# Performance work log

Measured on AMD Instinct MI355X. Metric: run time of the kernel, lower is better.

Reference implementation:

```python
import jax, jax.numpy as jnp
import numpy as np
from jax import lax

PRE_NMS_TOPK = 6000
POST_NMS_TOPK = 1000
NMS_THRESH = 0.7
MIN_SIZE = 16.0


def setup_inputs() -> dict:
    key = jax.random.key(0)
    k1, k2, k3, k4, k5 = jax.random.split(key, 5)
    B, N = 16, 200000
    # anchors: valid boxes (x1 < x2, y1 < y2) from random centers / sizes
    cxy = jax.random.uniform(k1, (B, N, 2), dtype=jnp.float32) * 1000.0
    wh = 16.0 + jax.random.uniform(k2, (B, N, 2), dtype=jnp.float32) * 284.0
    anchors = jnp.concatenate([cxy - 0.5 * wh, cxy + 0.5 * wh], axis=-1)  # [B,N,4] x1,y1,x2,y2
    image_sizes = jax.random.randint(k3, (B, 2), 512, 1024, dtype=jnp.int32)  # (h, w)
    objectness_logits = jax.random.normal(k4, (B, N, 1), dtype=jnp.float32)
    bbox_deltas = jax.random.normal(k5, (B, N, 4), dtype=jnp.float32) * 0.2
    return {"anchors": anchors, "image_sizes": image_sizes,
            "objectness_logits": objectness_logits, "bbox_deltas": bbox_deltas}


def _per_image(anchors, image_size, logits, deltas):
    # --- box decode ---
    a_w = anchors[:, 2] - anchors[:, 0]
    a_h = anchors[:, 3] - anchors[:, 1]
    a_x = anchors[:, 0] + 0.5 * a_w
    a_y = anchors[:, 1] + 0.5 * a_h
    p_x = a_x + deltas[:, 0] * a_w
    p_y = a_y + deltas[:, 1] * a_h
    p_w = a_w * jnp.exp(jnp.clip(deltas[:, 2], -10.0, 10.0))
    p_h = a_h * jnp.exp(jnp.clip(deltas[:, 3], -10.0, 10.0))
    h = image_size[0].astype(jnp.float32)
    w = image_size[1].astype(jnp.float32)
    x1 = jnp.clip(p_x - 0.5 * p_w, 0.0, w - 1.0)
    y1 = jnp.clip(p_y - 0.5 * p_h, 0.0, h - 1.0)
    x2 = jnp.clip(p_x + 0.5 * p_w, 0.0, w - 1.0)
    y2 = jnp.clip(p_y + 0.5 * p_h, 0.0, h - 1.0)
    proposals = jnp.stack([x1, y1, x2, y2], axis=1)  # [N,4]
    # --- min-size filter (mask instead of gather) ---
    valid = ((x2 - x1) >= MIN_SIZE) & ((y2 - y1) >= MIN_SIZE)
    fg = jax.nn.sigmoid(logits[:, 0])
    fg = jnp.where(valid, fg, -1.0)  # sentinel < 0 marks invalid
    # --- pre-NMS top-k ---
    scores, idx = lax.top_k(fg, PRE_NMS_TOPK)  # descending
    props = proposals[idx]  # [K,4]
    lgt = logits[idx]       # [K,1]
    dlt = deltas[idx]       # [K,4]
    bx1, by1, bx2, by2 = props[:, 0], props[:, 1], props[:, 2], props[:, 3]
    areas = (bx2 - bx1) * (by2 - by1)

    # --- greedy NMS: select highest remaining score, suppress IoU > thresh ---
    def step(sc, _):
        i = jnp.argmax(sc)
        s = sc[i]
        iw = jnp.maximum(0.0, jnp.minimum(bx2, bx2[i]) - jnp.maximum(bx1, bx1[i]))
        ih = jnp.maximum(0.0, jnp.minimum(by2, by2[i]) - jnp.maximum(by1, by1[i]))
        inter = iw * ih
        union = areas + areas[i] - inter
        iou = jnp.where(union > 0.0, inter / jnp.where(union > 0.0, union, 1.0), 0.0)
        sc = jnp.where(iou > NMS_THRESH, -1.0, sc)
        sc = sc.at[i].set(-1.0)
        return sc, (i, s > -0.5)

    _, (keep_idx, keep_valid) = lax.scan(step, scores, None, length=POST_NMS_TOPK)
    vm = keep_valid[:, None]
    out_p = jnp.where(vm, props[keep_idx], 0.0)
    out_l = jnp.where(vm, lgt[keep_idx], 1e-08)
    out_d = jnp.where(vm, dlt[keep_idx], 0.0)
    return out_p, out_l, out_d, keep_valid


def reference(anchors, image_sizes, objectness_logits, bbox_deltas):
    return jax.vmap(_per_image)(anchors, image_sizes, objectness_logits, bbox_deltas)
```

## Files before the change

### kernel.cpp

```cpp
#include <hip/hip_runtime.h>

#define BN 16
#define NN 200000
#define TOPK 6000
#define POSTK 1000
#define MW 285744
#define KEY_NEGHALF 0x40FFFFFFu
#define EQCAP 8192

#pragma clang fp contract(off)

typedef unsigned long long u64;

__device__ __forceinline__ float exp_cr(float x) {
  return (float)exp((double)x);
}

__device__ __forceinline__ unsigned key_of(float s) {
  unsigned u = __float_as_uint(s);
  return (u & 0x80000000u) ? ~u : (u | 0x80000000u);
}

__device__ __forceinline__ void decode_box(float4 a, float4 d, float W1, float H1,
                                           float& x1, float& y1, float& x2, float& y2,
                                           bool& valid) {
  float aw = a.z - a.x;
  float ah = a.w - a.y;
  float ax = a.x + 0.5f * aw;
  float ay = a.y + 0.5f * ah;
  float px = ax + d.x * aw;
  float py = ay + d.y * ah;
  float cz = fminf(fmaxf(d.z, -10.0f), 10.0f);
  float cw = fminf(fmaxf(d.w, -10.0f), 10.0f);
  float pw = aw * exp_cr(cz);
  float ph = ah * exp_cr(cw);
  x1 = fminf(fmaxf(px - 0.5f * pw, 0.0f), W1);
  y1 = fminf(fmaxf(py - 0.5f * ph, 0.0f), H1);
  x2 = fminf(fmaxf(px + 0.5f * pw, 0.0f), W1);
  y2 = fminf(fmaxf(py + 0.5f * ph, 0.0f), H1);
  valid = ((x2 - x1) >= 16.0f) && ((y2 - y1) >= 16.0f);
}

__device__ __forceinline__ float score_of(float lg, bool valid) {
  float e = exp_cr(-lg);
  float s = 1.0f / (1.0f + e);
  return valid ? s : -1.0f;
}

__global__ __launch_bounds__(256) void k_score(const float4* __restrict__ anchors,
                                               const int* __restrict__ isz,
                                               const float* __restrict__ logits,
                                               const float4* __restrict__ deltas,
                                               unsigned* __restrict__ keys,
                                               unsigned* __restrict__ hist0) {
  __shared__ unsigned h[256];
  int b = blockIdx.y;
  int idx = blockIdx.x * 256 + threadIdx.x;
  int lane = threadIdx.x & 63;
  h[threadIdx.x] = 0;
  __syncthreads();
  unsigned bin = 0;
  bool active = idx < NN;
  if (active) {
    size_t i = (size_t)b * NN + idx;
    float4 a = anchors[i];
    float4 d = deltas[i];
    float H1 = (float)isz[2 * b] - 1.0f;
    float W1 = (float)isz[2 * b + 1] - 1.0f;
    float x1, y1, x2, y2; bool valid;
    decode_box(a, d, W1, H1, x1, y1, x2, y2, valid);
    float sc = score_of(logits[i], valid);
    unsigned key = key_of(sc);
    keys[i] = key;
    bin = key >> 24;
  }
  u64 act = __ballot(active);
  while (act) {
    int l = __ffsll(act) - 1;
    unsigned vb = __shfl(bin, l);
    u64 same = __ballot(bin == vb) & act;
    if (lane == l) atomicAdd(&h[vb], (unsigned)__popcll(same));
    act &= ~same;
  }
  __syncthreads();
  unsigned c = h[threadIdx.x];
  if (c) atomicAdd(&hist0[((size_t)b * 8 + (blockIdx.x & 7)) * 256 + threadIdx.x], c);
}

__global__ void k_sel0(const unsigned* __restrict__ hist0, unsigned* __restrict__ meta) {
  int b = blockIdx.x, t = threadIdx.x;
  __shared__ unsigned c[256];
  unsigned s = 0;
  for (int sh = 0; sh < 8; ++sh) s += hist0[((size_t)b * 8 + sh) * 256 + t];
  c[t] = s;
  __syncthreads();
  if (t == 0) {
    unsigned cum = 0;
    for (int u = 255; u >= 0; --u) {
      if (cum + c[u] >= TOPK) { meta[b * 8 + 0] = (unsigned)u; meta[b * 8 + 1] = cum; break; }
      cum += c[u];
    }
  }
}

__global__ __launch_bounds__(256) void k_h1(const unsigned* __restrict__ keys,
                                            const unsigned* __restrict__ meta,
                                            unsigned* __restrict__ hist1) {
  int b = blockIdx.y;
  int idx = blockIdx.x * 256 + threadIdx.x;
  if (idx >= NN) return;
  unsigned key = keys[(size_t)b * NN + idx];
  unsigned B0 = meta[b * 8 + 0];
  if ((key >> 24) == B0)
    atomicAdd(&hist1[(size_t)b * 65536 + ((key >> 8) & 0xFFFFu)], 1u);
}

__global__ void k_sel1(const unsigned* __restrict__ hist1, unsigned* __restrict__ meta) {
  int b = blockIdx.x, t = threadIdx.x;
  __shared__ unsigned part[256];
  __shared__ unsigned above[256];
  const unsigned* h = hist1 + (size_t)b * 65536;
  unsigned cA0 = meta[b * 8 + 1];
  unsigned R1 = TOPK - cA0;
  int base = t * 256;
  unsigned sum = 0;
  for (int j = 0; j < 256; ++j) sum += h[base + j];
  part[t] = sum;
  __syncthreads();
  if (t == 0) {
    unsigned run = 0;
    for (int u = 255; u >= 0; --u) { above[u] = run; run += part[u]; }
  }
  __syncthreads();
  unsigned ab = above[t];
  if (ab < R1 && ab + part[t] >= R1) {
    unsigned cum = ab;
    for (int j = 255; j >= 0; --j) {
      unsigned c = h[base + j];
      if (cum + c >= R1) {
        meta[b * 8 + 2] = (unsigned)(base + j);
        meta[b * 8 + 3] = cA0 + cum;
        break;
      }
      cum += c;
    }
  }
}

__global__ __launch_bounds__(256) void k_h2(const unsigned* __restrict__ keys,
                                            const unsigned* __restrict__ meta,
                                            unsigned* __restrict__ hist2) {
  int b = blockIdx.y;
  int idx = blockIdx.x * 256 + threadIdx.x;
  if (idx >= NN) return;
  unsigned key = keys[(size_t)b * NN + idx];
  unsigned pref = (meta[b * 8 + 0] << 16) | meta[b * 8 + 2];
  if ((key >> 8) == pref)
    atomicAdd(&hist2[b * 256 + (key & 0xFFu)], 1u);
}

__global__ void k_sel2(const unsigned* __restrict__ hist2, unsigned* __restrict__ meta) {
  int b = blockIdx.x, t = threadIdx.x;
  __shared__ unsigned c[256];
  c[t] = hist2[b * 256 + t];
  __syncthreads();
  if (t == 0) {
    unsigned R2 = TOPK - meta[b * 8 + 3];
    unsigned cum = 0;
    for (int u = 255; u >= 0; --u) {
      if (cum + c[u] >= R2) {
        unsigned K = (meta[b * 8 + 0] << 24) | (meta[b * 8 + 2] << 8) | (unsigned)u;
        unsigned nG = meta[b * 8 + 3] + cum;
        meta[b * 8 + 4] = K;
        meta[b * 8 + 5] = nG;
        meta[b * 8 + 6] = TOPK - nG;
        break;
      }
      cum += c[u];
    }
  }
}

__global__ __launch_bounds__(256) void k_compact(const unsigned* __restrict__ keys,
                                                 const unsigned* __restrict__ meta,
                                                 unsigned* __restrict__ cntGt,
                                                 unsigned* __restrict__ sel,
                                                 unsigned* __restrict__ cntEq,
                                                 unsigned* __restrict__ eq) {
  __shared__ unsigned sc[256];
  __shared__ unsigned baseSh;
  int b = blockIdx.y, tid = threadIdx.x;
  const unsigned* kb = keys + (size_t)b * NN;
  unsigned K = meta[b * 8 + 4];
  int start = blockIdx.x * 8000;
  int end = start + 8000 < NN ? start + 8000 : NN;
  unsigned cnt = 0;
  for (int n = start + tid; n < end; n += 256) cnt += (kb[n] > K);
  sc[tid] = cnt;
  __syncthreads();
  if (tid == 0) {
    unsigned run = 0;
    for (int u = 0; u < 256; ++u) { unsigned v = sc[u]; sc[u] = run; run += v; }
    baseSh = run ? atomicAdd(&cntGt[b * 64], run) : 0u;
  }
  __syncthreads();
  unsigned pos = baseSh + sc[tid];
  for (int n = start + tid; n < end; n += 256) {
    unsigned kv = kb[n];
    if (kv > K) {
      sel[(size_t)b * TOPK + pos++] = (unsigned)n;
    } else if (kv == K) {
      unsigned p = atomicAdd(&cntEq[b * 64], 1u);
      if (p < EQCAP) eq[(size_t)b * EQCAP + p] = (unsigned)n;
    }
  }
}

__global__ __launch_bounds__(256) void k_resolve2(const unsigned* __restrict__ eq,
                                                  const unsigned* __restrict__ cntEq,
                                                  const unsigned* __restrict__ meta,
                                                  unsigned* __restrict__ sel) {
  __shared__ unsigned lst[EQCAP];
  int b = blockIdx.x, t = threadIdx.x;
  unsigned cnt = cntEq[b * 64];
  if (cnt > EQCAP) cnt = EQCAP;
  unsigned nG = meta[b * 8 + 5], nE = meta[b * 8 + 6];
  for (unsigned j = t; j < cnt; j += 256) lst[j] = eq[(size_t)b * EQCAP + j];
  __syncthreads();
  for (unsigned j = t; j < cnt; j += 256) {
    unsigned my = lst[j];
    unsigned rank = 0;
    for (unsigned k = 0; k < cnt; ++k) rank += (lst[k] < my);
    if (rank < nE) sel[(size_t)b * TOPK + nG + rank] = my;
  }
}

__global__ __launch_bounds__(1024) void k_sort(const float4* __restrict__ anchors,
                                               const int* __restrict__ isz,
                                               const unsigned* __restrict__ keys,
                                               const float4* __restrict__ deltas,
                                               const unsigned* __restrict__ sel,
                                               unsigned* __restrict__ sIdx,
                                               unsigned* __restrict__ sKey,
                                               float4* __restrict__ sBox,
                                               float* __restrict__ sAr) {
  __shared__ u64 skey[8192];
  int b = blockIdx.x, tid = threadIdx.x;
  for (int p = tid; p < 8192; p += 1024) {
    u64 kk = 0;
    if (p < TOPK) {
      unsigned n = sel[(size_t)b * TOPK + p];
      kk = ((u64)keys[(size_t)b * NN + n] << 32) | (unsigned)(NN - 1 - (int)n);
    }
    skey[p] = kk;
  }
  __syncthreads();
  for (unsigned k = 2; k <= 8192; k <<= 1) {
    for (unsigned j = k >> 1; j > 0; j >>= 1) {
      for (unsigned p = tid; p < 4096; p += 1024) {
        unsigned i = ((p & ~(j - 1)) << 1) | (p & (j - 1));
        unsigned x = i | j;
        u64 a = skey[i], c = skey[x];
        bool desc = ((i & k) == 0);
        if (desc ? (a < c) : (a > c)) { skey[i] = c; skey[x] = a; }
      }
      __syncthreads();
    }
  }
  float H1 = (float)isz[2 * b] - 1.0f;
  float W1 = (float)isz[2 * b + 1] - 1.0f;
  for (int i = tid; i < TOPK; i += 1024) {
    u64 kk = skey[i];
    unsigned n = (unsigned)(NN - 1) - (unsigned)(kk & 0xFFFFFFFFull);
    sIdx[(size_t)b * TOPK + i] = n;
    sKey[(size_t)b * TOPK + i] = (unsigned)(kk >> 32);
    float4 a = anchors[(size_t)b * NN + n];
    float4 d = deltas[(size_t)b * NN + n];
    float x1, y1, x2, y2; bool valid;
    decode_box(a, d, W1, H1, x1, y1, x2, y2, valid);
    sBox[(size_t)b * TOPK + i] = make_float4(x1, y1, x2, y2);
    sAr[(size_t)b * TOPK + i] = (x2 - x1) * (y2 - y1);
  }
}

__global__ __launch_bounds__(256) void k_iou(const float4* __restrict__ sBox,
                                             const float* __restrict__ sAr,
                                             u64* __restrict__ mat) {
  int Bk = blockIdx.x;
  int c = blockIdx.y;
  int b = blockIdx.z;
  int wlo = c * 16;
  int whi = wlo + 16 > 94 ? 94 : wlo + 16;
  if (wlo < Bk) wlo = Bk;
  if (wlo >= whi) return;
  int tid = threadIdx.x, wv = tid >> 6, lane = tid & 63;
  __shared__ float4 cb[1024];
  __shared__ float ca[1024];
  __shared__ float4 rb[64];
  __shared__ float ra[64];
  const float4* sb = sBox + (size_t)b * TOPK;
  const float* sa = sAr + (size_t)b * TOPK;
  for (int u = tid; u < 1024; u += 256) {
    int j = c * 1024 + u;
    int jc = j < TOPK ? j : TOPK - 1;
    cb[u] = sb[jc];
    ca[u] = sa[jc];
  }
  if (tid < 64) {
    int i = Bk * 64 + tid;
    int ic = i < TOPK ? i : TOPK - 1;
    rb[tid] = sb[ic];
    ra[tid] = sa[ic];
  }
  __syncthreads();
  const double T = (double)0.7f + 0x1p-25;
  size_t matb = (size_t)b * MW;
  for (int g = 0; g < 4; ++g) {
    int r0 = wv * 16 + g * 4;
    float4 r4[4]; float rar[4]; size_t ro[4]; bool rok[4];
    for (int k = 0; k < 4; ++k) {
      int i = Bk * 64 + r0 + k;
      r4[k] = rb[r0 + k];
      rar[k] = ra[r0 + k];
      rok[k] = i < TOPK;
      int rm = i & 63;
      ro[k] = matb + (size_t)(94 * i - (32 * Bk * (Bk - 1) + Bk * rm)) - (size_t)Bk;
    }
    for (int w = wlo; w < whi; ++w) {
      int u = (w - c * 16) * 64 + lane;
      float4 c4 = cb[u];
      float car = ca[u];
#pragma unroll
      for (int k = 0; k < 4; ++k) {
        if (!rok[k]) continue;
        float iw = fminf(c4.z, r4[k].z) - fmaxf(c4.x, r4[k].x);
        iw = fmaxf(iw, 0.0f);
        float ih = fminf(c4.w, r4[k].w) - fmaxf(c4.y, r4[k].y);
        ih = fmaxf(ih, 0.0f);
        float inter = iw * ih;
        float uni = (car + rar[k]) - inter;
        bool pred = (uni > 0.0f) && ((double)inter >= T * (double)uni);
        u64 w64 = __ballot(pred);
        if (lane == 0) mat[ro[k] + (size_t)w] = w64;
      }
    }
  }
}

__global__ __launch_bounds__(1024) void k_scan(const float4* __restrict__ anchors,
                                               const int* __restrict__ isz,
                                               const float* __restrict__ logits,
                                               const float4* __restrict__ deltas,
                                               const unsigned* __restrict__ sIdx,
                                               const unsigned* __restrict__ sKey,
                                               const u64* __restrict__ mat,
                                               float* __restrict__ out) {
  __shared__ u64 rmW[94];
  __shared__ u64 diagb[2][64];
  __shared__ unsigned keyb[2][64];
  __shared__ unsigned idxb[2][64];
  __shared__ unsigned keepL[POSTK];
  __shared__ unsigned picksList[64];
  __shared__ int nkSh, npicksSh, allInvSh;
  int b = blockIdx.x, tid = threadIdx.x, lane = tid & 63, wv = tid >> 6;
  const u64* mb = mat + (size_t)b * MW;
  const size_t bT = (size_t)b * TOPK;
  if (tid < 94) rmW[tid] = 0;
  if (tid == 0) { nkSh = 0; allInvSh = 0; }
  if (wv == 1) {
    diagb[0][lane] = mb[(size_t)(94 * lane)];
    keyb[0][lane] = sKey[bT + lane];
    idxb[0][lane] = sIdx[bT + lane];
  }
  __syncthreads();
  for (int B = 0; B < 94; ++B) {
    if (nkSh >= POSTK || allInvSh) break;
    int par = B & 1;
    if (wv == 0) {
      unsigned skl = keyb[par][lane];
      unsigned nl = idxb[par][lane];
      u64 w0 = diagb[par][lane];
      u64 v64 = __ballot(skl > KEY_NEGHALF);
      int base = nkSh;
      u64 alive = v64 & ~rmW[B];
      u64 picks = 0;
      int cnt = 0, lim = POSTK - base;
      while (alive && cnt < lim) {
        int c = __ffsll(alive) - 1;
        picks |= 1ull << c;
        ++cnt;
        u64 sup = __shfl(w0, c);
        alive &= ~sup;
        alive &= ~((2ull << c) - 1ull);
      }
      int rank = __popcll(picks & ((1ull << lane) - 1ull));
      if ((picks >> lane) & 1ull) {
        keepL[base + rank] = nl;
        picksList[rank] = (unsigned)lane;
      }
      if (lane == 0) { npicksSh = cnt; nkSh = base + cnt; allInvSh = (v64 == 0); }
    } else if (wv == 1) {
      int nb = B + 1;
      if (nb < 94) {
        int i2 = nb * 64 + lane;
        if (i2 < TOPK) {
          int off2 = 94 * i2 - 32 * nb * (nb - 1) - nb * lane;
          diagb[nb & 1][lane] = mb[(size_t)off2];
          keyb[nb & 1][lane] = sKey[bT + i2];
          idxb[nb & 1][lane] = sIdx[bT + i2];
        } else {
          diagb[nb & 1][lane] = 0;
          keyb[nb & 1][lane] = 0;
          idxb[nb & 1][lane] = 0;
        }
      }
    }
    __syncthreads();
    int np = npicksSh;
    if (tid >= 128 && np > 0) {
      int t = tid - 128;
      int w = B + 1 + (t >> 3);
      int k = t & 7;
      if (w < 94) {
        int base94 = 6016 * B - 32 * B * (B - 1);
        int span = 94 - B;
        u64 a0 = 0, a1 = 0;
        int j = k;
        for (; j + 8 < np; j += 16) {
          a0 |= mb[(size_t)(base94 + span * (int)picksList[j] + (w - B))];
          a1 |= mb[(size_t)(base94 + span * (int)picksList[j + 8] + (w - B))];
        }
        if (j < np) a0 |= mb[(size_t)(base94 + span * (int)picksList[j] + (w - B))];
        a0 |= a1;
        if (a0) atomicOr(&rmW[w], a0);
      }
    }
    __syncthreads();
  }
  int nkF = nkSh;
  float H1 = (float)isz[2 * b] - 1.0f;
  float W1 = (float)isz[2 * b + 1] - 1.0f;
  const size_t base = (size_t)b * NN;
  for (int q = tid; q < POSTK; q += 1024) {
    float px1 = 0.f, py1 = 0.f, px2 = 0.f, py2 = 0.f;
    float L = 1e-8f, d0 = 0.f, d1 = 0.f, d2 = 0.f, d3 = 0.f, V = 0.f;
    if (q < nkF) {
      unsigned n = keepL[q];
      float4 a = anchors[base + n];
      float4 d = deltas[base + n];
      float x1, y1, x2, y2; bool valid;
      decode_box(a, d, W1, H1, x1, y1, x2, y2, valid);
      px1 = x1; py1 = y1; px2 = x2; py2 = y2;
      L = logits[base + n];
      d0 = d.x; d1 = d.y; d2 = d.z; d3 = d.w;
      V = 1.0f;
    }
    size_t row = (size_t)b * POSTK + q;
    float* outP = out + row * 4;
    outP[0] = px1; outP[1] = py1; outP[2] = px2; outP[3] = py2;
    out[(size_t)BN * POSTK * 4 + row] = L;
    float* outD = out + (size_t)BN * POSTK * 5 + row * 4;
    outD[0] = d0; outD[1] = d1; outD[2] = d2; outD[3] = d3;
    out[(size_t)BN * POSTK * 9 + row] = V;
  }
}

extern "C" void kernel_launch(void* const* d_in, const int* in_sizes, int n_in,
                              void* d_out, int out_size, void* d_ws, size_t ws_size,
                              hipStream_t stream) {
  const float4* anchors = (const float4*)d_in[0];
  const int* isz = (const int*)d_in[1];
  const float* logits = (const float*)d_in[2];
  const float4* deltas = (const float4*)d_in[3];
  float* out = (float*)d_out;

  unsigned* W = (unsigned*)d_ws;
  unsigned* hist1 = W;
  unsigned* keys = W + 1048576;
  unsigned* hist0 = W + 4248576;
  unsigned* hist2 = W + 4281344;
  unsigned* cntGt = W + 4285440;
  unsigned* meta = W + 4286464;
  unsigned* cntEq = W + 4286592;
  unsigned* eq = W + 4287616;
  u64* mat = (u64*)d_ws;
  unsigned* T = W + 9143808;
  unsigned* sel = T;
  unsigned* sIdx = T + 96000;
  unsigned* sKey = T + 192000;
  float4* sBox = (float4*)(T + 288000);
  float* sAr = (float*)(T + 672000);

  hipMemsetAsync(hist1, 0, (size_t)1048576 * 4, stream);
  hipMemsetAsync(hist0, 0, (size_t)(32768 + 4096 + 1024 + 128 + 1024) * 4, stream);

  dim3 gN((NN + 255) / 256, BN);
  k_score<<<gN, 256, 0, stream>>>(anchors, isz, logits, deltas, keys, hist0);
  k_sel0<<<BN, 256, 0, stream>>>(hist0, meta);
  k_h1<<<gN, 256, 0, stream>>>(keys, meta, hist1);
  k_sel1<<<BN, 256, 0, stream>>>(hist1, meta);
  k_h2<<<gN, 256, 0, stream>>>(keys, meta, hist2);
  k_sel2<<<BN, 256, 0, stream>>>(hist2, meta);
  k_compact<<<dim3(25, BN), 256, 0, stream>>>(keys, meta, cntGt, sel, cntEq, eq);
  k_resolve2<<<BN, 256, 0, stream>>>(eq, cntEq, meta, sel);
  k_sort<<<BN, 1024, 0, stream>>>(anchors, isz, keys, deltas, sel, sIdx, sKey, sBox, sAr);
  k_iou<<<dim3(94, 6, BN), 256, 0, stream>>>(sBox, sAr, mat);
  k_scan<<<BN, 1024, 0, stream>>>(anchors, isz, logits, deltas, sIdx, sKey, mat, out);
}
```

Baseline: 643.2 us.

## Replace precomputed IoU bitmask matrix with on-the-fly NMS against kept boxes

Removes the full upper-triangular IoU bitmask kernel and the matrix-driven scan. A single per-image kernel now, for each 64-box block, tests each candidate against only the boxes already kept (at most 1000, held in shared memory), computes the in-block diagonal mask by shuffles, and then runs the greedy pick. This avoids computing and writing roughly 6000x6000 IoU bits per image and the global loads needed to read them back. In exchange the work becomes serial, with 16 blocks on 1024 threads each, and the cost per block grows with the number of boxes kept so far.

```diff
diff --git a/kernel.cpp b/kernel.cpp
--- a/kernel.cpp
+++ b/kernel.cpp
@@ -4,7 +4,6 @@
 #define NN 200000
 #define TOPK 6000
 #define POSTK 1000
-#define MW 285744
 #define KEY_NEGHALF 0x40FFFFFFu
 #define EQCAP 8192
 
@@ -283,159 +282,92 @@
   }
 }
 
-__global__ __launch_bounds__(256) void k_iou(const float4* __restrict__ sBox,
-                                             const float* __restrict__ sAr,
-                                             u64* __restrict__ mat) {
-  int Bk = blockIdx.x;
-  int c = blockIdx.y;
-  int b = blockIdx.z;
-  int wlo = c * 16;
-  int whi = wlo + 16 > 94 ? 94 : wlo + 16;
-  if (wlo < Bk) wlo = Bk;
-  if (wlo >= whi) return;
-  int tid = threadIdx.x, wv = tid >> 6, lane = tid & 63;
-  __shared__ float4 cb[1024];
-  __shared__ float ca[1024];
-  __shared__ float4 rb[64];
-  __shared__ float ra[64];
-  const float4* sb = sBox + (size_t)b * TOPK;
-  const float* sa = sAr + (size_t)b * TOPK;
-  for (int u = tid; u < 1024; u += 256) {
-    int j = c * 1024 + u;
-    int jc = j < TOPK ? j : TOPK - 1;
-    cb[u] = sb[jc];
-    ca[u] = sa[jc];
-  }
-  if (tid < 64) {
-    int i = Bk * 64 + tid;
-    int ic = i < TOPK ? i : TOPK - 1;
-    rb[tid] = sb[ic];
-    ra[tid] = sa[ic];
-  }
+__global__ __launch_bounds__(1024) void k_nms(const float4* __restrict__ sBox,
+                                              const float* __restrict__ sAr,
+                                              const unsigned* __restrict__ sIdx,
+                                              const unsigned* __restrict__ sKey,
+                                              const float4* __restrict__ anchors,
+                                              const int* __restrict__ isz,
+                                              const float* __restrict__ logits,
+                                              const float4* __restrict__ deltas,
+                                              float* __restrict__ out) {
+  __shared__ float kx1[POSTK], ky1[POSTK], kx2[POSTK], ky2[POSTK], kar[POSTK];
+  __shared__ unsigned keptPos[POSTK];
+  __shared__ u64 diagb[64];
+  __shared__ u64 suppSh;
+  __shared__ int nkSh, stopSh;
+  int b = blockIdx.x, tid = threadIdx.x, lane = tid & 63, wv = tid >> 6;
+  const size_t bT = (size_t)b * TOPK;
+  if (tid == 0) { nkSh = 0; stopSh = 0; }
   __syncthreads();
   const double T = (double)0.7f + 0x1p-25;
-  size_t matb = (size_t)b * MW;
-  for (int g = 0; g < 4; ++g) {
-    int r0 = wv * 16 + g * 4;
-    float4 r4[4]; float rar[4]; size_t ro[4]; bool rok[4];
-    for (int k = 0; k < 4; ++k) {
-      int i = Bk * 64 + r0 + k;
-      r4[k] = rb[r0 + k];
-      rar[k] = ra[r0 + k];
-      rok[k] = i < TOPK;
-      int rm = i & 63;
-      ro[k] = matb + (size_t)(94 * i - (32 * Bk * (Bk - 1) + Bk * rm)) - (size_t)Bk;
-    }
-    for (int w = wlo; w < whi; ++w) {
-      int u = (w - c * 16) * 64 + lane;
-      float4 c4 = cb[u];
-      float car = ca[u];
-#pragma unroll
-      for (int k = 0; k < 4; ++k) {
-        if (!rok[k]) continue;
-        float iw = fminf(c4.z, r4[k].z) - fmaxf(c4.x, r4[k].x);
-        iw = fmaxf(iw, 0.0f);
-        float ih = fminf(c4.w, r4[k].w) - fmaxf(c4.y, r4[k].y);
-        ih = fmaxf(ih, 0.0f);
-        float inter = iw * ih;
-        float uni = (car + rar[k]) - inter;
-        bool pred = (uni > 0.0f) && ((double)inter >= T * (double)uni);
-        u64 w64 = __ballot(pred);
-        if (lane == 0) mat[ro[k] + (size_t)w] = w64;
-      }
-    }
-  }
-}
-
-__global__ __launch_bounds__(1024) void k_scan(const float4* __restrict__ anchors,
-                                               const int* __restrict__ isz,
-                                               const float* __restrict__ logits,
-                                               const float4* __restrict__ deltas,
-                                               const unsigned* __restrict__ sIdx,
-                                               const unsigned* __restrict__ sKey,
-                                               const u64* __restrict__ mat,
-                                               float* __restrict__ out) {
-  __shared__ u64 rmW[94];
-  __shared__ u64 diagb[2][64];
-  __shared__ unsigned keyb[2][64];
-  __shared__ unsigned idxb[2][64];
-  __shared__ unsigned keepL[POSTK];
-  __shared__ unsigned picksList[64];
-  __shared__ int nkSh, npicksSh, allInvSh;
-  int b = blockIdx.x, tid = threadIdx.x, lane = tid & 63, wv = tid >> 6;
-  const u64* mb = mat + (size_t)b * MW;
-  const size_t bT = (size_t)b * TOPK;
-  if (tid < 94) rmW[tid] = 0;
-  if (tid == 0) { nkSh = 0; allInvSh = 0; }
-  if (wv == 1) {
-    diagb[0][lane] = mb[(size_t)(94 * lane)];
-    keyb[0][lane] = sKey[bT + lane];
-    idxb[0][lane] = sIdx[bT + lane];
-  }
-  __syncthreads();
   for (int B = 0; B < 94; ++B) {
-    if (nkSh >= POSTK || allInvSh) break;
-    int par = B & 1;
+    int pos = B * 64 + lane;
+    float cx1 = 0.f, cy1 = 0.f, cx2 = 0.f, cy2 = 0.f, car = 0.f;
+    unsigned ckey = 0;
+    if (pos < TOPK) {
+      float4 bb = sBox[bT + pos];
+      cx1 = bb.x; cy1 = bb.y; cx2 = bb.z; cy2 = bb.w;
+      car = sAr[bT + pos];
+      ckey = sKey[bT + pos];
+    }
+    int nk0 = nkSh;
+    if (tid == 0) suppSh = 0;
+    __syncthreads();
+    bool sup = false;
+    for (int k = wv; k < nk0; k += 16) {
+      float rx1 = kx1[k], ry1 = ky1[k], rx2 = kx2[k], ry2 = ky2[k], rar = kar[k];
+      float iw = fminf(cx2, rx2) - fmaxf(cx1, rx1);
+      iw = fmaxf(iw, 0.0f);
+      float ih = fminf(cy2, ry2) - fmaxf(cy1, ry1);
+      ih = fmaxf(ih, 0.0f);
+      float inter = iw * ih;
+      float uni = (car + rar) - inter;
+      sup = sup || ((uni > 0.0f) && ((double)inter >= T * (double)uni));
+    }
+    u64 wsup = __ballot(sup);
+    if (wsup && lane == 0) atomicOr(&suppSh, wsup);
+    for (int rr = 0; rr < 4; ++rr) {
+      int r = wv * 4 + rr;
+      float rx1 = __shfl(cx1, r), ry1 = __shfl(cy1, r);
+      float rx2 = __shfl(cx2, r), ry2 = __shfl(cy2, r);
+      float rar = __shfl(car, r);
+      float iw = fminf(cx2, rx2) - fmaxf(cx1, rx1);
+      iw = fmaxf(iw, 0.0f);
+      float ih = fminf(cy2, ry2) - fmaxf(cy1, ry1);
+      ih = fmaxf(ih, 0.0f);
+      float inter = iw * ih;
+      float uni = (car + rar) - inter;
+      bool pd = (uni > 0.0f) && ((double)inter >= T * (double)uni);
+      u64 dw = __ballot(pd);
+      if (lane == 0) diagb[r] = dw;
+    }
+    __syncthreads();
     if (wv == 0) {
-      unsigned skl = keyb[par][lane];
-      unsigned nl = idxb[par][lane];
-      u64 w0 = diagb[par][lane];
-      u64 v64 = __ballot(skl > KEY_NEGHALF);
-      int base = nkSh;
-      u64 alive = v64 & ~rmW[B];
+      u64 w0 = diagb[lane];
+      u64 v64 = __ballot(ckey > KEY_NEGHALF);
+      u64 alive = v64 & ~suppSh;
       u64 picks = 0;
-      int cnt = 0, lim = POSTK - base;
+      int cnt = 0, lim = POSTK - nk0;
       while (alive && cnt < lim) {
         int c = __ffsll(alive) - 1;
         picks |= 1ull << c;
         ++cnt;
-        u64 sup = __shfl(w0, c);
-        alive &= ~sup;
+        u64 s2 = __shfl(w0, c);
+        alive &= ~s2;
         alive &= ~((2ull << c) - 1ull);
       }
       int rank = __popcll(picks & ((1ull << lane) - 1ull));
       if ((picks >> lane) & 1ull) {
-        keepL[base + rank] = nl;
-        picksList[rank] = (unsigned)lane;
+        int slot = nk0 + rank;
+        kx1[slot] = cx1; ky1[slot] = cy1; kx2[slot] = cx2; ky2[slot] = cy2;
+        kar[slot] = car;
+        keptPos[slot] = (unsigned)pos;
       }
-      if (lane == 0) { npicksSh = cnt; nkSh = base + cnt; allInvSh = (v64 == 0); }
-    } else if (wv == 1) {
-      int nb = B + 1;
-      if (nb < 94) {
-        int i2 = nb * 64 + lane;
-        if (i2 < TOPK) {
-          int off2 = 94 * i2 - 32 * nb * (nb - 1) - nb * lane;
-          diagb[nb & 1][lane] = mb[(size_t)off2];
-          keyb[nb & 1][lane] = sKey[bT + i2];
-          idxb[nb & 1][lane] = sIdx[bT + i2];
-        } else {
-          diagb[nb & 1][lane] = 0;
-          keyb[nb & 1][lane] = 0;
-          idxb[nb & 1][lane] = 0;
-        }
-      }
+      if (lane == 0) { nkSh = nk0 + cnt; stopSh = (v64 == 0); }
     }
     __syncthreads();
-    int np = npicksSh;
-    if (tid >= 128 && np > 0) {
-      int t = tid - 128;
-      int w = B + 1 + (t >> 3);
-      int k = t & 7;
-      if (w < 94) {
-        int base94 = 6016 * B - 32 * B * (B - 1);
-        int span = 94 - B;
-        u64 a0 = 0, a1 = 0;
-        int j = k;
-        for (; j + 8 < np; j += 16) {
-          a0 |= mb[(size_t)(base94 + span * (int)picksList[j] + (w - B))];
-          a1 |= mb[(size_t)(base94 + span * (int)picksList[j + 8] + (w - B))];
-        }
-        if (j < np) a0 |= mb[(size_t)(base94 + span * (int)picksList[j] + (w - B))];
-        a0 |= a1;
-        if (a0) atomicOr(&rmW[w], a0);
-      }
-    }
-    __syncthreads();
+    if (nkSh >= POSTK || stopSh) break;
   }
   int nkF = nkSh;
   float H1 = (float)isz[2 * b] - 1.0f;
@@ -445,7 +377,7 @@
     float px1 = 0.f, py1 = 0.f, px2 = 0.f, py2 = 0.f;
     float L = 1e-8f, d0 = 0.f, d1 = 0.f, d2 = 0.f, d3 = 0.f, V = 0.f;
     if (q < nkF) {
-      unsigned n = keepL[q];
+      unsigned n = sIdx[bT + keptPos[q]];
       float4 a = anchors[base + n];
       float4 d = deltas[base + n];
       float x1, y1, x2, y2; bool valid;
@@ -483,7 +415,6 @@
   unsigned* meta = W + 4286464;
   unsigned* cntEq = W + 4286592;
   unsigned* eq = W + 4287616;
-  u64* mat = (u64*)d_ws;
   unsigned* T = W + 9143808;
   unsigned* sel = T;
   unsigned* sIdx = T + 96000;
@@ -504,6 +435,5 @@
   k_compact<<<dim3(25, BN), 256, 0, stream>>>(keys, meta, cntGt, sel, cntEq, eq);
   k_resolve2<<<BN, 256, 0, stream>>>(eq, cntEq, meta, sel);
   k_sort<<<BN, 1024, 0, stream>>>(anchors, isz, keys, deltas, sel, sIdx, sKey, sBox, sAr);
-  k_iou<<<dim3(94, 6, BN), 256, 0, stream>>>(sBox, sAr, mat);
-  k_scan<<<BN, 1024, 0, stream>>>(anchors, isz, logits, deltas, sIdx, sKey, mat, out);
-}
+  k_nms<<<BN, 1024, 0, stream>>>(sBox, sAr, sIdx, sKey, anchors, isz, logits, deltas, out);
+}
```

After: 627.7 us. 1.02x faster.
